# Performance work log

Hardware: AMD Instinct MI355X
Metric: run time of the kernel (lower is better)

Reference implementation:

```python
import jax, jax.numpy as jnp
import numpy as np

N = 20000
IN_FT, HID1, HID2, OUT_FT = 256, 400, 200, 128
E = 320000


def gcn_layer(x, W, b, src, dst, ew, n_nodes):
    # PyG GCNConv: add self-loops (weight 1), symmetric normalization, then
    # propagate src -> dst (aggregate at edge_index[1]).
    loop = jnp.arange(n_nodes, dtype=src.dtype)
    s = jnp.concatenate([src, loop])
    d = jnp.concatenate([dst, loop])
    w = jnp.concatenate([ew, jnp.ones((n_nodes,), dtype=ew.dtype)])
    deg = jax.ops.segment_sum(w, d, num_segments=n_nodes)  # [N]
    dinv = jnp.where(deg > 0, jax.lax.rsqrt(jnp.where(deg > 0, deg, 1.0)), 0.0)
    norm = dinv[s] * w * dinv[d]                            # [E+N]
    h = x @ W                                               # [N, F_out]
    msgs = h[s] * norm[:, None]                             # gather + scale
    out = jax.ops.segment_sum(msgs, d, num_segments=n_nodes)
    return out + b


def setup_inputs() -> dict:
    key = jax.random.key(0)
    ks = jax.random.split(key, 10)
    x = jax.random.normal(ks[0], (N, IN_FT), dtype=jnp.float32)
    edge_index = jax.random.randint(ks[1], (2, E), 0, N, dtype=jnp.int64)
    edge_attr = jax.random.uniform(ks[2], (E,), dtype=jnp.float32)
    sc = lambda fin: 1.0 / np.sqrt(fin)
    fc_W = jax.random.uniform(ks[3], (IN_FT, HID1), jnp.float32, -sc(IN_FT), sc(IN_FT))
    fc_b = jax.random.uniform(ks[4], (HID1,), jnp.float32, -sc(IN_FT), sc(IN_FT))
    W1 = jax.random.uniform(ks[5], (HID1, HID2), jnp.float32, -sc(HID1), sc(HID1))
    b1 = jnp.zeros((HID2,), jnp.float32)
    W2 = jax.random.uniform(ks[6], (HID2, OUT_FT), jnp.float32, -sc(HID2), sc(HID2))
    b2 = jnp.zeros((OUT_FT,), jnp.float32)
    return {"x": x, "edge_index": edge_index, "edge_attr": edge_attr,
            "fc_W": fc_W, "fc_b": fc_b, "W1": W1, "b1": b1, "W2": W2, "b2": b2}


def reference(x, edge_index, edge_attr, fc_W, fc_b, W1, b1, W2, b2):
    src, dst = edge_index[0], edge_index[1]
    h = jax.nn.relu(x @ fc_W + fc_b)                 # Linear + ReLU
    h = jax.nn.relu(gcn_layer(h, W1, b1, src, dst, edge_attr, N))
    h = gcn_layer(h, W2, b2, src, dst, edge_attr, N)
    return jax.nn.relu(h)
```

## Files before the change

### kernel.cpp

```cpp
#include <hip/hip_runtime.h>


typedef unsigned short us;

namespace {
constexpr int NN = 20000;
constexpr int NE = 320000;
constexpr int IN_FT = 256, HID1 = 400, HID2 = 200, OUT_FT = 128;
constexpr int K1P = 448;
constexpr int K2P = 256;
constexpr int SBLK = 80;
constexpr int SCHUNK = 250;
using short8v = __attribute__((ext_vector_type(8))) short;
using f32x4 = __attribute__((ext_vector_type(4))) float;
}

__device__ __forceinline__ us f2bf(float f) {
  unsigned int u = __float_as_uint(f);
  u += 0x7FFFu + ((u >> 16) & 1u);
  return (us)(u >> 16);
}
__device__ __forceinline__ float bf2f(us h) {
  return __uint_as_float(((unsigned int)h) << 16);
}

__global__ __launch_bounds__(256) void zero_kernel(float4* __restrict__ p, int n4) {
  int i = blockIdx.x * 256 + threadIdx.x;
  if (i < n4) p[i] = make_float4(0.f, 0.f, 0.f, 0.f);
}

__global__ __launch_bounds__(256) void deg_count_kernel(const int* __restrict__ dst,
                                                        const float* __restrict__ ew,
                                                        float* __restrict__ deg,
                                                        int* __restrict__ cnt) {
  int tid = blockIdx.x * 256 + threadIdx.x;
  if (tid < NE) {
    int d = dst[tid];
    unsafeAtomicAdd(&deg[d], ew[tid]);
    atomicAdd(&cnt[d], 1);
  } else if (tid < NE + NN) {
    unsafeAtomicAdd(&deg[tid - NE], 1.0f);
  }
}

__global__ __launch_bounds__(256) void blocksum_dinv_kernel(const int* __restrict__ count,
                                                            int* __restrict__ bsum,
                                                            float* __restrict__ deg) {
  __shared__ int sdata[256];
  const int b = blockIdx.x, t = threadIdx.x;
  const int base = b * SCHUNK;
  int v = 0;
  if (t < SCHUNK) {
    const int i = base + t;
    v = count[i];
    float d = deg[i];
    deg[i] = d > 0.f ? rsqrtf(d) : 0.f;
  }
  sdata[t] = v;
  __syncthreads();
#pragma unroll
  for (int off = 128; off > 0; off >>= 1) {
    if (t < off) sdata[t] += sdata[t + off];
    __syncthreads();
  }
  if (t == 0) bsum[b] = sdata[0];
}

__global__ __launch_bounds__(128) void scanb_kernel(const int* __restrict__ bsum,
                                                    int* __restrict__ bpre) {
  __shared__ int s[SBLK];
  const int t = threadIdx.x;
  if (t < SBLK) s[t] = bsum[t];
  __syncthreads();
  for (int off = 1; off < SBLK; off <<= 1) {
    int v = 0;
    if (t < SBLK && t >= off) v = s[t - off];
    __syncthreads();
    if (t < SBLK && t >= off) s[t] += v;
    __syncthreads();
  }
  if (t < SBLK) bpre[t] = s[t] - bsum[t];
}

__global__ __launch_bounds__(256) void rowptr_kernel(const int* __restrict__ bpre,
                                                     int* __restrict__ count,
                                                     int* __restrict__ rowptr) {
  __shared__ int s[256];
  const int b = blockIdx.x, t = threadIdx.x;
  const int base = b * SCHUNK;
  const int v = (t < SCHUNK) ? count[base + t] : 0;
  s[t] = v;
  __syncthreads();
#pragma unroll
  for (int off = 1; off < 256; off <<= 1) {
    int u = 0;
    if (t >= off) u = s[t - off];
    __syncthreads();
    if (t >= off) s[t] += u;
    __syncthreads();
  }
  const int excl = s[t] - v + bpre[b];
  if (t < SCHUNK) {
    rowptr[base + t] = excl;
    count[base + t] = excl;
  }
  if (b == SBLK - 1 && t == 0) rowptr[NN] = NE;
}

__global__ __launch_bounds__(256) void scatter_kernel(const int* __restrict__ src,
                                                      const int* __restrict__ dst,
                                                      const float* __restrict__ ew,
                                                      const float* __restrict__ dinv,
                                                      int* __restrict__ fill,
                                                      int* __restrict__ srcS,
                                                      float* __restrict__ wS) {
  int e = blockIdx.x * 256 + threadIdx.x;
  if (e >= NE) return;
  int s = src[e], d = dst[e];
  int pos = atomicAdd(&fill[d], 1);
  srcS[pos] = s;
  wS[pos] = dinv[s] * ew[e] * dinv[d];
}

__global__ __launch_bounds__(256) void prep_kernel(
    const float* __restrict__ x, us* __restrict__ xh, us* __restrict__ xl,
    const float* __restrict__ fcW, const float* __restrict__ W1,
    const float* __restrict__ W2,
    us* __restrict__ fcWTh, us* __restrict__ fcWTl,
    us* __restrict__ W1Th, us* __restrict__ W1Tl,
    us* __restrict__ W2Th, us* __restrict__ W2Tl) {
  constexpr int NXS = NN * IN_FT / 8;
  constexpr int N0 = HID1 * IN_FT;
  constexpr int N1 = HID2 * K1P;
  constexpr int N2 = OUT_FT * K2P;
  int idx = blockIdx.x * 256 + threadIdx.x;
  if (idx < NXS) {
    const float4 v0 = reinterpret_cast<const float4*>(x)[idx * 2];
    const float4 v1 = reinterpret_cast<const float4*>(x)[idx * 2 + 1];
    const float v[8] = {v0.x, v0.y, v0.z, v0.w, v1.x, v1.y, v1.z, v1.w};
    short8v h, l;
#pragma unroll
    for (int j = 0; j < 8; ++j) {
      us hh = f2bf(v[j]);
      h[j] = (short)hh;
      l[j] = (short)f2bf(v[j] - bf2f(hh));
    }
    reinterpret_cast<short8v*>(xh)[idx] = h;
    reinterpret_cast<short8v*>(xl)[idx] = l;
    return;
  }
  int widx = idx - NXS;
  float v;
  us *th, *tl;
  int o;
  if (widx < N0) {
    o = widx;
    int n = o / IN_FT, k = o - n * IN_FT;
    v = fcW[(size_t)k * HID1 + n];
    th = fcWTh; tl = fcWTl;
  } else if (widx < N0 + N1) {
    o = widx - N0;
    int n = o / K1P, k = o - n * K1P;
    v = (k < HID1) ? W1[(size_t)k * HID2 + n] : 0.f;
    th = W1Th; tl = W1Tl;
  } else if (widx < N0 + N1 + N2) {
    o = widx - N0 - N1;
    int n = o / K2P, k = o - n * K2P;
    v = (k < HID2) ? W2[(size_t)k * OUT_FT + n] : 0.f;
    th = W2Th; tl = W2Tl;
  } else {
    return;
  }
  us h = f2bf(v);
  th[o] = h;
  tl[o] = f2bf(v - bf2f(h));
}

template <int KAP, bool BIAS, bool RELU, bool SPLIT>
__global__ __launch_bounds__(256) void gemm64_kernel(
    const us* __restrict__ Ah, const us* __restrict__ Al,
    const us* __restrict__ BTh, const us* __restrict__ BTl,
    const float* __restrict__ bias, float* __restrict__ Cf,
    us* __restrict__ Ch, us* __restrict__ Cl,
    int M, int N, int NPAD) {
  constexpr int BK = 64;
  constexpr int LDK = BK + 4;
  __shared__ us Ash[64][LDK];
  __shared__ us Asl[64][LDK];
  __shared__ us Bsh[64][LDK];
  __shared__ us Bsl[64][LDK];
  const int tid = threadIdx.x;
  const int lane = tid & 63;
  const int wid = tid >> 6;
  const int wm = wid >> 1, wn = wid & 1;
  const int m0 = blockIdx.y * 64, n0 = blockIdx.x * 64;
  const int sr = tid >> 2, sko = (tid & 3) * 16;
  const int arow = m0 + sr;
  const int brow = n0 + sr;
  const int l15 = lane & 15, kg = lane >> 4;
  const short8v zv = {0, 0, 0, 0, 0, 0, 0, 0};

  f32x4 acc[2][2];
#pragma unroll
  for (int i = 0; i < 2; ++i)
#pragma unroll
    for (int j = 0; j < 2; ++j)
#pragma unroll
      for (int c = 0; c < 4; ++c) acc[i][j][c] = 0.f;

  short8v pa0h, pa1h, pa0l, pa1l, pb0h, pb1h, pb0l, pb1l;
  auto gload = [&](int k0) {
    pa0h = pa1h = pa0l = pa1l = zv;
    pb0h = pb1h = pb0l = pb1l = zv;
    if (arow < M) {
      const size_t off = (size_t)arow * KAP + k0 + sko;
      pa0h = *reinterpret_cast<const short8v*>(Ah + off);
      pa1h = *reinterpret_cast<const short8v*>(Ah + off + 8);
      pa0l = *reinterpret_cast<const short8v*>(Al + off);
      pa1l = *reinterpret_cast<const short8v*>(Al + off + 8);
    }
    if (brow < N) {
      const size_t off = (size_t)brow * KAP + k0 + sko;
      pb0h = *reinterpret_cast<const short8v*>(BTh + off);
      pb1h = *reinterpret_cast<const short8v*>(BTh + off + 8);
      pb0l = *reinterpret_cast<const short8v*>(BTl + off);
      pb1l = *reinterpret_cast<const short8v*>(BTl + off + 8);
    }
  };
  auto sstore = [&]() {
    *reinterpret_cast<short8v*>(&Ash[sr][sko]) = pa0h;
    *reinterpret_cast<short8v*>(&Ash[sr][sko + 8]) = pa1h;
    *reinterpret_cast<short8v*>(&Asl[sr][sko]) = pa0l;
    *reinterpret_cast<short8v*>(&Asl[sr][sko + 8]) = pa1l;
    *reinterpret_cast<short8v*>(&Bsh[sr][sko]) = pb0h;
    *reinterpret_cast<short8v*>(&Bsh[sr][sko + 8]) = pb1h;
    *reinterpret_cast<short8v*>(&Bsl[sr][sko]) = pb0l;
    *reinterpret_cast<short8v*>(&Bsl[sr][sko + 8]) = pb1l;
  };

  gload(0);
  sstore();
  __syncthreads();
#pragma unroll
  for (int k0 = 0; k0 < KAP; k0 += BK) {
    const bool more = (k0 + BK < KAP);
    if (more) gload(k0 + BK);
#pragma unroll
    for (int kc = 0; kc < BK; kc += 32) {
      short8v afh[2], afl[2], bfh[2], bfl[2];
#pragma unroll
      for (int mf = 0; mf < 2; ++mf) {
        const int r = wm * 32 + mf * 16 + l15;
        afh[mf] = *reinterpret_cast<const short8v*>(&Ash[r][kc + kg * 8]);
        afl[mf] = *reinterpret_cast<const short8v*>(&Asl[r][kc + kg * 8]);
      }
#pragma unroll
      for (int nf = 0; nf < 2; ++nf) {
        const int c = wn * 32 + nf * 16 + l15;
        bfh[nf] = *reinterpret_cast<const short8v*>(&Bsh[c][kc + kg * 8]);
        bfl[nf] = *reinterpret_cast<const short8v*>(&Bsl[c][kc + kg * 8]);
      }
#pragma unroll
      for (int mf = 0; mf < 2; ++mf)
#pragma unroll
        for (int nf = 0; nf < 2; ++nf) {
          acc[mf][nf] = __builtin_amdgcn_mfma_f32_16x16x32_bf16(afh[mf], bfh[nf], acc[mf][nf], 0, 0, 0);
          acc[mf][nf] = __builtin_amdgcn_mfma_f32_16x16x32_bf16(afh[mf], bfl[nf], acc[mf][nf], 0, 0, 0);
          acc[mf][nf] = __builtin_amdgcn_mfma_f32_16x16x32_bf16(afl[mf], bfh[nf], acc[mf][nf], 0, 0, 0);
        }
    }
    __syncthreads();
    if (more) {
      sstore();
      __syncthreads();
    }
  }

#pragma unroll
  for (int nf = 0; nf < 2; ++nf) {
    const int col = n0 + wn * 32 + nf * 16 + l15;
    float bb = 0.f;
    if (BIAS && col < N) bb = bias[col];
#pragma unroll
    for (int mf = 0; mf < 2; ++mf) {
      const int rbase = m0 + wm * 32 + mf * 16 + kg * 4;
#pragma unroll
      for (int i = 0; i < 4; ++i) {
        const int row = rbase + i;
        if (row >= M) continue;
        if (col < N) {
          float v = acc[mf][nf][i];
          if (BIAS) v += bb;
          if (RELU) v = fmaxf(v, 0.f);
          if (SPLIT) {
            us h = f2bf(v);
            Ch[(size_t)row * NPAD + col] = h;
            Cl[(size_t)row * NPAD + col] = f2bf(v - bf2f(h));
          } else {
            Cf[(size_t)row * N + col] = v;
          }
        } else if (SPLIT && col < NPAD) {
          Ch[(size_t)row * NPAD + col] = 0;
          Cl[(size_t)row * NPAD + col] = 0;
        }
      }
    }
  }
}

template <int F, int OST, int NPW, bool SPLIT>
__global__ __launch_bounds__(256) void agg_gather_kernel(const int* __restrict__ rowptr,
                                                         const int* __restrict__ srcS,
                                                         const float* __restrict__ wS,
                                                         const float* __restrict__ t,
                                                         const float* __restrict__ dinv,
                                                         const float* __restrict__ bias,
                                                         float* __restrict__ out,
                                                         us* __restrict__ oh,
                                                         us* __restrict__ ol) {
  constexpr int LPN = F / 4;
  constexpr int LPNP = OST / 4;
  const int wv = threadIdx.x >> 6;
  const int lane = threadIdx.x & 63;
  const int sub = (NPW == 2) ? (lane >> 5) : 0;
  const int l = (NPW == 2) ? (lane & 31) : lane;
  const int node = blockIdx.x * (4 * NPW) + wv * NPW + sub;
  if (node >= NN) return;
  if (l >= LPN) {
    if (SPLIT && l < LPNP) {
      ushort4 z = make_ushort4(0, 0, 0, 0);
      *reinterpret_cast<ushort4*>(oh + (size_t)node * OST + l * 4) = z;
      *reinterpret_cast<ushort4*>(ol + (size_t)node * OST + l * 4) = z;
    }
    return;
  }
  const int beg = rowptr[node], end = rowptr[node + 1];
  const size_t fo = (size_t)l * 4;
  float4 acc0 = make_float4(0.f, 0.f, 0.f, 0.f);
  float4 acc1 = make_float4(0.f, 0.f, 0.f, 0.f);
  int j = beg;
  for (; j + 1 < end; j += 2) {
    const int s0 = srcS[j], s1 = srcS[j + 1];
    const float w0 = wS[j], w1 = wS[j + 1];
    const float4 v0 = *reinterpret_cast<const float4*>(t + (size_t)s0 * F + fo);
    const float4 v1 = *reinterpret_cast<const float4*>(t + (size_t)s1 * F + fo);
    acc0.x = fmaf(v0.x, w0, acc0.x); acc0.y = fmaf(v0.y, w0, acc0.y);
    acc0.z = fmaf(v0.z, w0, acc0.z); acc0.w = fmaf(v0.w, w0, acc0.w);
    acc1.x = fmaf(v1.x, w1, acc1.x); acc1.y = fmaf(v1.y, w1, acc1.y);
    acc1.z = fmaf(v1.z, w1, acc1.z); acc1.w = fmaf(v1.w, w1, acc1.w);
  }
  if (j < end) {
    const int s0 = srcS[j];
    const float w0 = wS[j];
    const float4 v0 = *reinterpret_cast<const float4*>(t + (size_t)s0 * F + fo);
    acc0.x = fmaf(v0.x, w0, acc0.x); acc0.y = fmaf(v0.y, w0, acc0.y);
    acc0.z = fmaf(v0.z, w0, acc0.z); acc0.w = fmaf(v0.w, w0, acc0.w);
  }
  const float di = dinv[node];
  const float sw = di * di;
  const float4 tv = *reinterpret_cast<const float4*>(t + (size_t)node * F + fo);
  const float4 bb = *reinterpret_cast<const float4*>(bias + fo);
  float4 o;
  o.x = fmaxf(fmaf(tv.x, sw, acc0.x + acc1.x) + bb.x, 0.f);
  o.y = fmaxf(fmaf(tv.y, sw, acc0.y + acc1.y) + bb.y, 0.f);
  o.z = fmaxf(fmaf(tv.z, sw, acc0.z + acc1.z) + bb.z, 0.f);
  o.w = fmaxf(fmaf(tv.w, sw, acc0.w + acc1.w) + bb.w, 0.f);
  if (SPLIT) {
    ushort4 hv, lv;
    hv.x = f2bf(o.x); lv.x = f2bf(o.x - bf2f(hv.x));
    hv.y = f2bf(o.y); lv.y = f2bf(o.y - bf2f(hv.y));
    hv.z = f2bf(o.z); lv.z = f2bf(o.z - bf2f(hv.z));
    hv.w = f2bf(o.w); lv.w = f2bf(o.w - bf2f(hv.w));
    *reinterpret_cast<ushort4*>(oh + (size_t)node * OST + fo) = hv;
    *reinterpret_cast<ushort4*>(ol + (size_t)node * OST + fo) = lv;
  } else {
    *reinterpret_cast<float4*>(out + (size_t)node * F + fo) = o;
  }
}

extern "C" void kernel_launch(void* const* d_in, const int* in_sizes, int n_in,
                              void* d_out, int out_size, void* d_ws, size_t ws_size,
                              hipStream_t stream) {
  const float* x = (const float*)d_in[0];
  const int* ei = (const int*)d_in[1];
  const float* ea = (const float*)d_in[2];
  const float* fcW = (const float*)d_in[3];
  const float* fcb = (const float*)d_in[4];
  const float* W1 = (const float*)d_in[5];
  const float* b1 = (const float*)d_in[6];
  const float* W2 = (const float*)d_in[7];
  const float* b2 = (const float*)d_in[8];
  const int* srcIdx = ei;
  const int* dstIdx = ei + NE;

  char* ws = (char*)d_ws;
  constexpr size_t KB_ = 1u << 10;
  float* dinv = (float*)(ws);
  int* cnt = (int*)(ws + 80000);
  int* rowptr = (int*)(ws + 160000);
  int* bsum = (int*)(ws + 244 * KB_);
  int* bpre = (int*)(ws + 245 * KB_);
  int* srcS = (int*)(ws + 256 * KB_);
  float* wS = (float*)(ws + 1536 * KB_);
  us* fcWTh = (us*)(ws + 2880 * KB_);
  us* fcWTl = (us*)(ws + 3088 * KB_);
  us* W1Th = (us*)(ws + 3296 * KB_);
  us* W1Tl = (us*)(ws + 3472 * KB_);
  us* W2Th = (us*)(ws + 3648 * KB_);
  us* W2Tl = (us*)(ws + 3712 * KB_);
  us* xh = (us*)(ws + 3776 * KB_);
  us* xl = (us*)(ws + 13784 * KB_);
  us* h1h = (us*)(ws + 23800 * KB_);
  us* h1l = (us*)(ws + 41350 * KB_);
  float* t1 = (float*)(ws + 3776 * KB_);
  us* h2h = (us*)(ws + 23800 * KB_);
  us* h2l = (us*)(ws + 33800 * KB_);
  float* t2 = (float*)(ws + 3776 * KB_);

  zero_kernel<<<(40000 / 4 + 255) / 256, 256, 0, stream>>>((float4*)ws, 40000 / 4);
  deg_count_kernel<<<(NE + NN + 255) / 256, 256, 0, stream>>>(dstIdx, ea, dinv, cnt);
  blocksum_dinv_kernel<<<SBLK, 256, 0, stream>>>(cnt, bsum, dinv);
  scanb_kernel<<<1, 128, 0, stream>>>(bsum, bpre);
  rowptr_kernel<<<SBLK, 256, 0, stream>>>(bpre, cnt, rowptr);
  scatter_kernel<<<(NE + 255) / 256, 256, 0, stream>>>(srcIdx, dstIdx, ea, dinv, cnt, srcS, wS);

  {
    constexpr int TOT = NN * IN_FT / 8 + HID1 * IN_FT + HID2 * K1P + OUT_FT * K2P;
    prep_kernel<<<(TOT + 255) / 256, 256, 0, stream>>>(
        x, xh, xl, fcW, W1, W2, fcWTh, fcWTl, W1Th, W1Tl, W2Th, W2Tl);
  }

  const int MBLK = (NN + 63) / 64;

  gemm64_kernel<IN_FT, true, true, true><<<dim3((HID1 + 63) / 64, MBLK), 256, 0, stream>>>(
      xh, xl, fcWTh, fcWTl, fcb, nullptr, h1h, h1l, NN, HID1, K1P);

  gemm64_kernel<K1P, false, false, false><<<dim3((HID2 + 63) / 64, MBLK), 256, 0, stream>>>(
      h1h, h1l, W1Th, W1Tl, nullptr, t1, nullptr, nullptr, NN, HID2, HID2);
  agg_gather_kernel<HID2, K2P, 1, true><<<(NN + 3) / 4, 256, 0, stream>>>(
      rowptr, srcS, wS, t1, dinv, b1, nullptr, h2h, h2l);

  gemm64_kernel<K2P, false, false, false><<<dim3((OUT_FT + 63) / 64, MBLK), 256, 0, stream>>>(
      h2h, h2l, W2Th, W2Tl, nullptr, t2, nullptr, nullptr, NN, OUT_FT, OUT_FT);
  agg_gather_kernel<OUT_FT, OUT_FT, 2, false><<<(NN + 7) / 8, 256, 0, stream>>>(
      rowptr, srcS, wS, t2, dinv, b2, (float*)d_out, nullptr, nullptr);
}
```

Measured before the change: 214.7 us.

## Fuse graph preprocessing and weight prep into one cooperative kernel with grid syncs

Replaces seven small launches (zero, degree count, block sums, block scan, rowptr scan, edge scatter, input/weight bf16 split) with a single cooperative kernel of 512 blocks that uses grid.sync between phases. The x/weight conversion is overlapped with the degree-atomic phase, and the two-level scan drops its separate single-block kernel by having each block sum preceding block totals directly. This cuts launch overhead and inter-kernel gaps, but grid-strided loops over a fixed 512-block grid and the grid-wide barriers may lower per-phase throughput.

```diff
diff --git a/kernel.cpp b/kernel.cpp
--- a/kernel.cpp
+++ b/kernel.cpp
@@ -1,6 +1,8 @@
 #include <hip/hip_runtime.h>
-
-
+#include <hip/hip_cooperative_groups.h>
+
+
+namespace cg = cooperative_groups;
 typedef unsigned short us;
 
 namespace {
@@ -11,6 +13,28 @@
 constexpr int K2P = 256;
 constexpr int SBLK = 80;
 constexpr int SCHUNK = 250;
+constexpr int FGRID = 512;
+constexpr int NXS = NN * IN_FT / 8;
+constexpr int NW = HID1 * IN_FT + HID2 * K1P + OUT_FT * K2P;
+constexpr size_t OFF_DINV = 0;
+constexpr size_t OFF_CNT = 80000;
+constexpr size_t OFF_ROWPTR = 160000;
+constexpr size_t OFF_BSUM = 244u << 10;
+constexpr size_t OFF_SRCS = 256u << 10;
+constexpr size_t OFF_WSW = 1536u << 10;
+constexpr size_t OFF_FCWTH = 2880u << 10;
+constexpr size_t OFF_FCWTL = 3088u << 10;
+constexpr size_t OFF_W1TH = 3296u << 10;
+constexpr size_t OFF_W1TL = 3472u << 10;
+constexpr size_t OFF_W2TH = 3648u << 10;
+constexpr size_t OFF_W2TL = 3712u << 10;
+constexpr size_t OFF_XH = 3776u << 10;
+constexpr size_t OFF_XL = 13784u << 10;
+constexpr size_t OFF_H1H = 23800u << 10;
+constexpr size_t OFF_H1L = 41350u << 10;
+constexpr size_t OFF_T = 3776u << 10;
+constexpr size_t OFF_H2H = 23800u << 10;
+constexpr size_t OFF_H2L = 33800u << 10;
 using short8v = __attribute__((ext_vector_type(8))) short;
 using f32x4 = __attribute__((ext_vector_type(4))) float;
 }
@@ -24,119 +48,48 @@
   return __uint_as_float(((unsigned int)h) << 16);
 }
 
-__global__ __launch_bounds__(256) void zero_kernel(float4* __restrict__ p, int n4) {
-  int i = blockIdx.x * 256 + threadIdx.x;
-  if (i < n4) p[i] = make_float4(0.f, 0.f, 0.f, 0.f);
-}
-
-__global__ __launch_bounds__(256) void deg_count_kernel(const int* __restrict__ dst,
-                                                        const float* __restrict__ ew,
-                                                        float* __restrict__ deg,
-                                                        int* __restrict__ cnt) {
-  int tid = blockIdx.x * 256 + threadIdx.x;
-  if (tid < NE) {
-    int d = dst[tid];
-    unsafeAtomicAdd(&deg[d], ew[tid]);
-    atomicAdd(&cnt[d], 1);
-  } else if (tid < NE + NN) {
-    unsafeAtomicAdd(&deg[tid - NE], 1.0f);
-  }
-}
-
-__global__ __launch_bounds__(256) void blocksum_dinv_kernel(const int* __restrict__ count,
-                                                            int* __restrict__ bsum,
-                                                            float* __restrict__ deg) {
+__global__ __launch_bounds__(256) void fused_front_kernel(
+    const int* __restrict__ ei, const float* __restrict__ ea,
+    const float* __restrict__ x, const float* __restrict__ fcW,
+    const float* __restrict__ W1, const float* __restrict__ W2,
+    char* __restrict__ ws) {
+  cg::grid_group grid = cg::this_grid();
+  const int* srcIdx = ei;
+  const int* dstIdx = ei + NE;
+  float* dinv = (float*)(ws + OFF_DINV);
+  int* cnt = (int*)(ws + OFF_CNT);
+  int* rowptr = (int*)(ws + OFF_ROWPTR);
+  int* bsum = (int*)(ws + OFF_BSUM);
+  int* srcS = (int*)(ws + OFF_SRCS);
+  float* wS = (float*)(ws + OFF_WSW);
+  us* xh = (us*)(ws + OFF_XH);
+  us* xl = (us*)(ws + OFF_XL);
+  us* fcWTh = (us*)(ws + OFF_FCWTH);
+  us* fcWTl = (us*)(ws + OFF_FCWTL);
+  us* W1Th = (us*)(ws + OFF_W1TH);
+  us* W1Tl = (us*)(ws + OFF_W1TL);
+  us* W2Th = (us*)(ws + OFF_W2TH);
+  us* W2Tl = (us*)(ws + OFF_W2TL);
+
+  const int gid = blockIdx.x * 256 + threadIdx.x;
+  const int gsz = FGRID * 256;
   __shared__ int sdata[256];
-  const int b = blockIdx.x, t = threadIdx.x;
-  const int base = b * SCHUNK;
-  int v = 0;
-  if (t < SCHUNK) {
-    const int i = base + t;
-    v = count[i];
-    float d = deg[i];
-    deg[i] = d > 0.f ? rsqrtf(d) : 0.f;
-  }
-  sdata[t] = v;
-  __syncthreads();
-#pragma unroll
-  for (int off = 128; off > 0; off >>= 1) {
-    if (t < off) sdata[t] += sdata[t + off];
-    __syncthreads();
-  }
-  if (t == 0) bsum[b] = sdata[0];
-}
-
-__global__ __launch_bounds__(128) void scanb_kernel(const int* __restrict__ bsum,
-                                                    int* __restrict__ bpre) {
-  __shared__ int s[SBLK];
-  const int t = threadIdx.x;
-  if (t < SBLK) s[t] = bsum[t];
-  __syncthreads();
-  for (int off = 1; off < SBLK; off <<= 1) {
-    int v = 0;
-    if (t < SBLK && t >= off) v = s[t - off];
-    __syncthreads();
-    if (t < SBLK && t >= off) s[t] += v;
-    __syncthreads();
-  }
-  if (t < SBLK) bpre[t] = s[t] - bsum[t];
-}
-
-__global__ __launch_bounds__(256) void rowptr_kernel(const int* __restrict__ bpre,
-                                                     int* __restrict__ count,
-                                                     int* __restrict__ rowptr) {
-  __shared__ int s[256];
-  const int b = blockIdx.x, t = threadIdx.x;
-  const int base = b * SCHUNK;
-  const int v = (t < SCHUNK) ? count[base + t] : 0;
-  s[t] = v;
-  __syncthreads();
-#pragma unroll
-  for (int off = 1; off < 256; off <<= 1) {
-    int u = 0;
-    if (t >= off) u = s[t - off];
-    __syncthreads();
-    if (t >= off) s[t] += u;
-    __syncthreads();
-  }
-  const int excl = s[t] - v + bpre[b];
-  if (t < SCHUNK) {
-    rowptr[base + t] = excl;
-    count[base + t] = excl;
-  }
-  if (b == SBLK - 1 && t == 0) rowptr[NN] = NE;
-}
-
-__global__ __launch_bounds__(256) void scatter_kernel(const int* __restrict__ src,
-                                                      const int* __restrict__ dst,
-                                                      const float* __restrict__ ew,
-                                                      const float* __restrict__ dinv,
-                                                      int* __restrict__ fill,
-                                                      int* __restrict__ srcS,
-                                                      float* __restrict__ wS) {
-  int e = blockIdx.x * 256 + threadIdx.x;
-  if (e >= NE) return;
-  int s = src[e], d = dst[e];
-  int pos = atomicAdd(&fill[d], 1);
-  srcS[pos] = s;
-  wS[pos] = dinv[s] * ew[e] * dinv[d];
-}
-
-__global__ __launch_bounds__(256) void prep_kernel(
-    const float* __restrict__ x, us* __restrict__ xh, us* __restrict__ xl,
-    const float* __restrict__ fcW, const float* __restrict__ W1,
-    const float* __restrict__ W2,
-    us* __restrict__ fcWTh, us* __restrict__ fcWTl,
-    us* __restrict__ W1Th, us* __restrict__ W1Tl,
-    us* __restrict__ W2Th, us* __restrict__ W2Tl) {
-  constexpr int NXS = NN * IN_FT / 8;
-  constexpr int N0 = HID1 * IN_FT;
-  constexpr int N1 = HID2 * K1P;
-  constexpr int N2 = OUT_FT * K2P;
-  int idx = blockIdx.x * 256 + threadIdx.x;
-  if (idx < NXS) {
-    const float4 v0 = reinterpret_cast<const float4*>(x)[idx * 2];
-    const float4 v1 = reinterpret_cast<const float4*>(x)[idx * 2 + 1];
+
+  for (int i = gid; i < 40000; i += gsz) ((int*)ws)[i] = 0;
+  grid.sync();
+
+  for (int t = gid; t < NE + NN; t += gsz) {
+    if (t < NE) {
+      int d = dstIdx[t];
+      unsafeAtomicAdd(&dinv[d], ea[t]);
+      atomicAdd(&cnt[d], 1);
+    } else {
+      unsafeAtomicAdd(&dinv[t - NE], 1.0f);
+    }
+  }
+  for (int i = gid; i < NXS; i += gsz) {
+    const float4 v0 = reinterpret_cast<const float4*>(x)[i * 2];
+    const float4 v1 = reinterpret_cast<const float4*>(x)[i * 2 + 1];
     const float v[8] = {v0.x, v0.y, v0.z, v0.w, v1.x, v1.y, v1.z, v1.w};
     short8v h, l;
 #pragma unroll
@@ -145,35 +98,93 @@
       h[j] = (short)hh;
       l[j] = (short)f2bf(v[j] - bf2f(hh));
     }
-    reinterpret_cast<short8v*>(xh)[idx] = h;
-    reinterpret_cast<short8v*>(xl)[idx] = l;
-    return;
-  }
-  int widx = idx - NXS;
-  float v;
-  us *th, *tl;
-  int o;
-  if (widx < N0) {
-    o = widx;
-    int n = o / IN_FT, k = o - n * IN_FT;
-    v = fcW[(size_t)k * HID1 + n];
-    th = fcWTh; tl = fcWTl;
-  } else if (widx < N0 + N1) {
-    o = widx - N0;
-    int n = o / K1P, k = o - n * K1P;
-    v = (k < HID1) ? W1[(size_t)k * HID2 + n] : 0.f;
-    th = W1Th; tl = W1Tl;
-  } else if (widx < N0 + N1 + N2) {
-    o = widx - N0 - N1;
-    int n = o / K2P, k = o - n * K2P;
-    v = (k < HID2) ? W2[(size_t)k * OUT_FT + n] : 0.f;
-    th = W2Th; tl = W2Tl;
-  } else {
-    return;
-  }
-  us h = f2bf(v);
-  th[o] = h;
-  tl[o] = f2bf(v - bf2f(h));
+    reinterpret_cast<short8v*>(xh)[i] = h;
+    reinterpret_cast<short8v*>(xl)[i] = l;
+  }
+  for (int widx = gid; widx < NW; widx += gsz) {
+    constexpr int N0 = HID1 * IN_FT;
+    constexpr int N1 = HID2 * K1P;
+    float v;
+    us *th, *tl;
+    int o;
+    if (widx < N0) {
+      o = widx;
+      int n = o / IN_FT, k = o - n * IN_FT;
+      v = fcW[(size_t)k * HID1 + n];
+      th = fcWTh; tl = fcWTl;
+    } else if (widx < N0 + N1) {
+      o = widx - N0;
+      int n = o / K1P, k = o - n * K1P;
+      v = (k < HID1) ? W1[(size_t)k * HID2 + n] : 0.f;
+      th = W1Th; tl = W1Tl;
+    } else {
+      o = widx - N0 - N1;
+      int n = o / K2P, k = o - n * K2P;
+      v = (k < HID2) ? W2[(size_t)k * OUT_FT + n] : 0.f;
+      th = W2Th; tl = W2Tl;
+    }
+    us h = f2bf(v);
+    th[o] = h;
+    tl[o] = f2bf(v - bf2f(h));
+  }
+  grid.sync();
+
+  for (int i = gid; i < NN; i += gsz) {
+    float d = dinv[i];
+    dinv[i] = d > 0.f ? rsqrtf(d) : 0.f;
+  }
+  if (blockIdx.x < SBLK) {
+    const int base = blockIdx.x * SCHUNK;
+    int v = (threadIdx.x < SCHUNK) ? cnt[base + threadIdx.x] : 0;
+    sdata[threadIdx.x] = v;
+    __syncthreads();
+#pragma unroll
+    for (int off = 128; off > 0; off >>= 1) {
+      if (threadIdx.x < off) sdata[threadIdx.x] += sdata[threadIdx.x + off];
+      __syncthreads();
+    }
+    if (threadIdx.x == 0) bsum[blockIdx.x] = sdata[0];
+  }
+  grid.sync();
+
+  if (blockIdx.x < SBLK) {
+    int contrib = (threadIdx.x < blockIdx.x) ? bsum[threadIdx.x] : 0;
+    sdata[threadIdx.x] = contrib;
+    __syncthreads();
+#pragma unroll
+    for (int off = 128; off > 0; off >>= 1) {
+      if (threadIdx.x < off) sdata[threadIdx.x] += sdata[threadIdx.x + off];
+      __syncthreads();
+    }
+    const int bpre = sdata[0];
+    __syncthreads();
+    const int base = blockIdx.x * SCHUNK;
+    const int v = (threadIdx.x < SCHUNK) ? cnt[base + threadIdx.x] : 0;
+    sdata[threadIdx.x] = v;
+    __syncthreads();
+#pragma unroll
+    for (int off = 1; off < 256; off <<= 1) {
+      int u = 0;
+      if (threadIdx.x >= off) u = sdata[threadIdx.x - off];
+      __syncthreads();
+      if (threadIdx.x >= off) sdata[threadIdx.x] += u;
+      __syncthreads();
+    }
+    const int excl = sdata[threadIdx.x] - v + bpre;
+    if (threadIdx.x < SCHUNK) {
+      rowptr[base + threadIdx.x] = excl;
+      cnt[base + threadIdx.x] = excl;
+    }
+    if (blockIdx.x == 0 && threadIdx.x == 0) rowptr[NN] = NE;
+  }
+  grid.sync();
+
+  for (int e = gid; e < NE; e += gsz) {
+    int s = srcIdx[e], d = dstIdx[e];
+    int pos = atomicAdd(&cnt[d], 1);
+    srcS[pos] = s;
+    wS[pos] = dinv[s] * ea[e] * dinv[d];
+  }
 }
 
 template <int KAP, bool BIAS, bool RELU, bool SPLIT>
@@ -390,44 +401,32 @@
   const float* b1 = (const float*)d_in[6];
   const float* W2 = (const float*)d_in[7];
   const float* b2 = (const float*)d_in[8];
-  const int* srcIdx = ei;
-  const int* dstIdx = ei + NE;
 
   char* ws = (char*)d_ws;
-  constexpr size_t KB_ = 1u << 10;
-  float* dinv = (float*)(ws);
-  int* cnt = (int*)(ws + 80000);
-  int* rowptr = (int*)(ws + 160000);
-  int* bsum = (int*)(ws + 244 * KB_);
-  int* bpre = (int*)(ws + 245 * KB_);
-  int* srcS = (int*)(ws + 256 * KB_);
-  float* wS = (float*)(ws + 1536 * KB_);
-  us* fcWTh = (us*)(ws + 2880 * KB_);
-  us* fcWTl = (us*)(ws + 3088 * KB_);
-  us* W1Th = (us*)(ws + 3296 * KB_);
-  us* W1Tl = (us*)(ws + 3472 * KB_);
-  us* W2Th = (us*)(ws + 3648 * KB_);
-  us* W2Tl = (us*)(ws + 3712 * KB_);
-  us* xh = (us*)(ws + 3776 * KB_);
-  us* xl = (us*)(ws + 13784 * KB_);
-  us* h1h = (us*)(ws + 23800 * KB_);
-  us* h1l = (us*)(ws + 41350 * KB_);
-  float* t1 = (float*)(ws + 3776 * KB_);
-  us* h2h = (us*)(ws + 23800 * KB_);
-  us* h2l = (us*)(ws + 33800 * KB_);
-  float* t2 = (float*)(ws + 3776 * KB_);
-
-  zero_kernel<<<(40000 / 4 + 255) / 256, 256, 0, stream>>>((float4*)ws, 40000 / 4);
-  deg_count_kernel<<<(NE + NN + 255) / 256, 256, 0, stream>>>(dstIdx, ea, dinv, cnt);
-  blocksum_dinv_kernel<<<SBLK, 256, 0, stream>>>(cnt, bsum, dinv);
-  scanb_kernel<<<1, 128, 0, stream>>>(bsum, bpre);
-  rowptr_kernel<<<SBLK, 256, 0, stream>>>(bpre, cnt, rowptr);
-  scatter_kernel<<<(NE + 255) / 256, 256, 0, stream>>>(srcIdx, dstIdx, ea, dinv, cnt, srcS, wS);
+  float* dinv = (float*)(ws + OFF_DINV);
+  int* rowptr = (int*)(ws + OFF_ROWPTR);
+  int* srcS = (int*)(ws + OFF_SRCS);
+  float* wS = (float*)(ws + OFF_WSW);
+  us* fcWTh = (us*)(ws + OFF_FCWTH);
+  us* fcWTl = (us*)(ws + OFF_FCWTL);
+  us* W1Th = (us*)(ws + OFF_W1TH);
+  us* W1Tl = (us*)(ws + OFF_W1TL);
+  us* W2Th = (us*)(ws + OFF_W2TH);
+  us* W2Tl = (us*)(ws + OFF_W2TL);
+  us* xh = (us*)(ws + OFF_XH);
+  us* xl = (us*)(ws + OFF_XL);
+  us* h1h = (us*)(ws + OFF_H1H);
+  us* h1l = (us*)(ws + OFF_H1L);
+  float* t1 = (float*)(ws + OFF_T);
+  us* h2h = (us*)(ws + OFF_H2H);
+  us* h2l = (us*)(ws + OFF_H2L);
+  float* t2 = (float*)(ws + OFF_T);
 
   {
-    constexpr int TOT = NN * IN_FT / 8 + HID1 * IN_FT + HID2 * K1P + OUT_FT * K2P;
-    prep_kernel<<<(TOT + 255) / 256, 256, 0, stream>>>(
-        x, xh, xl, fcW, W1, W2, fcWTh, fcWTl, W1Th, W1Tl, W2Th, W2Tl);
+    void* kargs[] = {(void*)&ei, (void*)&ea, (void*)&x, (void*)&fcW,
+                     (void*)&W1, (void*)&W2, (void*)&ws};
+    hipLaunchCooperativeKernel((void*)fused_front_kernel, dim3(FGRID), dim3(256),
+                               kargs, 0, stream);
   }
 
   const int MBLK = (NN + 63) / 64;
```

Result: slower. 419.5 us (+95.3%).
